# Kernel tuning notes

Hardware: AMD Instinct MI355X
Metric: run time of the kernel (lower is better)

Reference implementation:

```python
import jax, jax.numpy as jnp
import numpy as np

D, H, DFF, NE, ND, B = 512, 8, 2048, 64, 64, 16

def _ln(x, g, b):
    m = x.mean(-1, keepdims=True)
    v = ((x - m) ** 2).mean(-1, keepdims=True)
    return (x - m) * jax.lax.rsqrt(v + 1e-5) * g + b

def _mha(q, k, v, Wi, bi, Wo, bo, h=H):
    # q,k,v: (L, B, d) seq-first, like torch nn.MultiheadAttention (eval mode)
    Lq, Bb, d = q.shape
    hd = d // h
    Wq, Wk, Wv = jnp.split(Wi, 3, axis=0)
    bq, bk, bv = jnp.split(bi, 3)
    def proj(x, W, bb):
        y = x @ W.T + bb                                  # (L, B, d)
        return y.reshape(x.shape[0], Bb, h, hd).transpose(1, 2, 0, 3)  # (B, h, L, hd)
    qh = proj(q, Wq, bq) * (hd ** -0.5)
    kh = proj(k, Wk, bk)
    vh = proj(v, Wv, bv)
    a = jax.nn.softmax(jnp.einsum('bhqe,bhke->bhqk', qh, kh), axis=-1)
    o = jnp.einsum('bhqk,bhke->bhqe', a, vh).transpose(2, 0, 1, 3).reshape(Lq, Bb, d)
    return o @ Wo.T + bo

def _ffn(x, W1, b1, W2, b2):
    return jax.nn.relu(x @ W1.T + b1) @ W2.T + b2

def _forward(enc, dec, ec_Wi, ec_bi, ec_Wo, ec_bo, dc_Wi, dc_bi, dc_Wo, dc_bo,
             es_Wi, es_bi, es_Wo, es_bo, ds_Wi, ds_bi, ds_Wo, ds_bo,
             eff_W1, eff_b1, eff_W2, eff_b2, dff_W1, dff_b1, dff_W2, dff_b2,
             n_ec_g, n_ec_b, n_es_g, n_es_b, n_ef_g, n_ef_b, n_dc_g, n_dc_b,
             n_dci_g, n_dci_b, n_ds_g, n_ds_b, n_df_g, n_df_b, pW, pWb, pv, pb):
    f_n = _ln(enc, n_ec_g, n_ec_b)   # (ne, B, d) -- normed once, reused for all j
    G_n = _ln(dec, n_dc_g, n_dc_b)   # (nd, B, d)
    # dec_cross for all j at once (key/value is the single token f_j)
    dc_out = jax.vmap(lambda fj: _mha(G_n, fj[None], fj[None], dc_Wi, dc_bi, dc_Wo, dc_bo))(f_n)  # (ne, nd, B, d)
    G_fj = dec[None] + dc_out                            # (ne, nd, B, d)
    G_im = _ln(G_fj, n_dci_g, n_dci_b)
    # enc_cross for all j at once (query is the single token f_j)
    ec_out = jax.vmap(lambda fj, Gj: _mha(fj[None], Gj, Gj, ec_Wi, ec_bi, ec_Wo, ec_bo)[0])(f_n, G_im)  # (ne, B, d)
    enc1 = enc + ec_out
    # attention pooling over the ne fusion copies
    G_c = G_fj.transpose(2, 1, 0, 3)                     # (B, nd, ne, d)
    energy = jnp.tanh(G_c @ pW.T + pWb + pb)
    w = jax.nn.softmax(energy @ pv.T, axis=2)            # (B, nd, ne, 1)
    dec1 = (G_c * w).sum(axis=2).transpose(1, 0, 2)      # (nd, B, d)
    # self-attention + FFN (pre-norm residual)
    en = _ln(enc1, n_es_g, n_es_b)
    enc2 = enc1 + _mha(en, en, en, es_Wi, es_bi, es_Wo, es_bo)
    dn = _ln(dec1, n_ds_g, n_ds_b)
    dec2 = dec1 + _mha(dn, dn, dn, ds_Wi, ds_bi, ds_Wo, ds_bo)
    enc3 = enc2 + _ffn(_ln(enc2, n_ef_g, n_ef_b), eff_W1, eff_b1, eff_W2, eff_b2)
    dec3 = dec2 + _ffn(_ln(dec2, n_df_g, n_df_b), dff_W1, dff_b1, dff_W2, dff_b2)
    return (enc3, dec3)

def setup_inputs() -> dict:
    key = jax.random.key(0)
    ks = iter(jax.random.split(key, 64))
    def w(shape, scale=0.05):
        return jax.random.normal(next(ks), shape, jnp.float32) * scale
    d, dff = D, DFF
    inp = {
        'enc': jax.random.normal(next(ks), (NE, B, d), jnp.float32),
        'dec': jax.random.normal(next(ks), (ND, B, d), jnp.float32),
    }
    for p in ['ec', 'dc', 'es', 'ds']:
        inp[p + '_Wi'] = w((3 * d, d)); inp[p + '_bi'] = jnp.zeros(3 * d, jnp.float32)
        inp[p + '_Wo'] = w((d, d)); inp[p + '_bo'] = jnp.zeros(d, jnp.float32)
    for p in ['eff', 'dff']:
        inp[p + '_W1'] = w((dff, d)); inp[p + '_b1'] = jnp.zeros(dff, jnp.float32)
        inp[p + '_W2'] = w((d, dff)); inp[p + '_b2'] = jnp.zeros(d, jnp.float32)
    for p in ['n_ec', 'n_es', 'n_ef', 'n_dc', 'n_dci', 'n_ds', 'n_df']:
        inp[p + '_g'] = jnp.ones(d, jnp.float32); inp[p + '_b'] = jnp.zeros(d, jnp.float32)
    inp['pW'] = w((d, d)); inp['pWb'] = jnp.zeros(d, jnp.float32)
    inp['pv'] = w((1, d)); inp['pb'] = jnp.zeros(d, jnp.float32)
    return inp

def reference(enc, dec, ec_Wi, ec_bi, ec_Wo, ec_bo, dc_Wi, dc_bi, dc_Wo, dc_bo,
              es_Wi, es_bi, es_Wo, es_bo, ds_Wi, ds_bi, ds_Wo, ds_bo,
              eff_W1, eff_b1, eff_W2, eff_b2, dff_W1, dff_b1, dff_W2, dff_b2,
              n_ec_g, n_ec_b, n_es_g, n_es_b, n_ef_g, n_ef_b, n_dc_g, n_dc_b,
              n_dci_g, n_dci_b, n_ds_g, n_ds_b, n_df_g, n_df_b, pW, pWb, pv, pb):
    return _forward(enc, dec, ec_Wi, ec_bi, ec_Wo, ec_bo, dc_Wi, dc_bi, dc_Wo, dc_bo,
                    es_Wi, es_bi, es_Wo, es_bo, ds_Wi, ds_bi, ds_Wo, ds_bo,
                    eff_W1, eff_b1, eff_W2, eff_b2, dff_W1, dff_b1, dff_W2, dff_b2,
                    n_ec_g, n_ec_b, n_es_g, n_es_b, n_ef_g, n_ef_b, n_dc_g, n_dc_b,
                    n_dci_g, n_dci_b, n_ds_g, n_ds_b, n_df_g, n_df_b, pW, pWb, pv, pb)
```

## Files before the change

### kernel.cpp

```cpp
#include <hip/hip_runtime.h>


typedef __bf16 bf16_t;
typedef bf16_t bf16x8 __attribute__((ext_vector_type(8)));
typedef float f32x4 __attribute__((ext_vector_type(4)));
typedef unsigned short u16x4 __attribute__((ext_vector_type(4)));
typedef unsigned short u16x8 __attribute__((ext_vector_type(8)));

__device__ inline unsigned short f2bf(float f) {
  unsigned int u = __float_as_uint(f);
  u += 0x7fffu + ((u >> 16) & 1u);
  return (unsigned short)(u >> 16);
}
__device__ inline float bf2f(unsigned short u) {
  return __uint_as_float(((unsigned int)u) << 16);
}

__device__ inline float wsum(float v) {
#pragma unroll
  for (int o = 1; o < 64; o <<= 1) v += __shfl_xor(v, o);
  return v;
}
__device__ inline float wmax(float v) {
#pragma unroll
  for (int o = 1; o < 64; o <<= 1) v = fmaxf(v, __shfl_xor(v, o));
  return v;
}

struct CastJob {
  const float* src;
  unsigned short* dst;
  int n;
  const float* cs;
};
struct CastPage {
  const float* src;
  unsigned short* dst;
};

__device__ inline void ln_body(const float* __restrict__ x,
                               const float* __restrict__ g,
                               const float* __restrict__ be,
                               unsigned short* __restrict__ y, int t) {
  float2 v = *(const float2*)(x + 2 * t);
  float s = wsum(v.x + v.y);
  float s2 = wsum(v.x * v.x + v.y * v.y);
  __shared__ float sh[8];
  int w = t >> 6, lane = t & 63;
  if (lane == 0) { sh[w] = s; sh[4 + w] = s2; }
  __syncthreads();
  s = sh[0] + sh[1] + sh[2] + sh[3];
  s2 = sh[4] + sh[5] + sh[6] + sh[7];
  float mean = s * (1.f / 512.f);
  float var = s2 * (1.f / 512.f) - mean * mean;
  float r = rsqrtf(var + 1e-5f);
  float2 gg = *(const float2*)(g + 2 * t);
  float2 bb = *(const float2*)(be + 2 * t);
  unsigned int pk = (unsigned int)f2bf((v.x - mean) * r * gg.x + bb.x) |
                    ((unsigned int)f2bf((v.y - mean) * r * gg.y + bb.y) << 16);
  *(unsigned int*)(y + 2 * t) = pk;
}

__device__ inline void stats_body(const float* __restrict__ x,
                                  float* __restrict__ m, float* __restrict__ q2,
                                  unsigned short* __restrict__ xb, int t,
                                  int row) {
  float2 v = *(const float2*)(x + 2 * t);
  if (xb) {
    unsigned int pk = (unsigned int)f2bf(v.x) | ((unsigned int)f2bf(v.y) << 16);
    *(unsigned int*)(xb + 2 * t) = pk;
  }
  float s = wsum(v.x + v.y);
  float s2 = wsum(v.x * v.x + v.y * v.y);
  __shared__ float sh2[8];
  int w = t >> 6, lane = t & 63;
  if (lane == 0) { sh2[w] = s; sh2[4 + w] = s2; }
  __syncthreads();
  if (t == 0) {
    s = sh2[0] + sh2[1] + sh2[2] + sh2[3];
    s2 = sh2[4] + sh2[5] + sh2[6] + sh2[7];
    m[row] = s * (1.f / 512.f);
    q2[row] = s2 * (1.f / 512.f);
  }
}

struct Phase0Args {
  const float* enc; const float* g_ec; const float* b_ec; unsigned short* f_n;
  const float* dec; float* md; float* q2d; unsigned short* dec_b;
  CastJob cast[4];
  const float* Wk; const float* Wv; const float* bk; const float* bv;
  const float* g_dci; const float* b_dci;
  float* u_k; float* u_v; float* c_k; float* c_v;
  const float* WoA; const float* WvA; unsigned short* Wfb;
  const float* bv2; const float* bo2; float* bf_out;
  float* zbase; int zcount;
};

__global__ __launch_bounds__(256) void phase0(Phase0Args a) {
  __shared__ unsigned short WAs[64][72];
  __shared__ unsigned short WBs[64][72];
  int bx = blockIdx.x;
  const int t = threadIdx.x;
  if (bx < 64) {
    const int bm = (bx >> 3) * 64;
    const int bn = (bx & 7) * 64;
    const int lane = t & 63;
    const int wave = t >> 6;
    const int wr = wave >> 1;
    const int wc = wave & 1;
    const int fr = lane & 15;
    const int fg = lane >> 4;
    const int rr = t >> 2;
    const int c = (t & 3) * 16;
    f32x4 acc[2][2] = {};
    for (int m0 = 0; m0 < 512; m0 += 64) {
      const float* ap = a.WoA + (size_t)(bm + rr) * 512 + m0 + c;
      float4 a0 = *(const float4*)ap;
      float4 a1 = *(const float4*)(ap + 4);
      float4 a2 = *(const float4*)(ap + 8);
      float4 a3 = *(const float4*)(ap + 12);
      u16x8 lo = {f2bf(a0.x), f2bf(a0.y), f2bf(a0.z), f2bf(a0.w),
                  f2bf(a1.x), f2bf(a1.y), f2bf(a1.z), f2bf(a1.w)};
      u16x8 hi = {f2bf(a2.x), f2bf(a2.y), f2bf(a2.z), f2bf(a2.w),
                  f2bf(a3.x), f2bf(a3.y), f2bf(a3.z), f2bf(a3.w)};
      *(u16x8*)&WAs[rr][c] = lo;
      *(u16x8*)&WAs[rr][c + 8] = hi;
      const float* bp = a.WvA + (size_t)(m0 + rr) * 512 + bn + c;
      float4 b0 = *(const float4*)bp;
      float4 b1 = *(const float4*)(bp + 4);
      float4 b2 = *(const float4*)(bp + 8);
      float4 b3 = *(const float4*)(bp + 12);
      float bv16[16] = {b0.x, b0.y, b0.z, b0.w, b1.x, b1.y, b1.z, b1.w,
                        b2.x, b2.y, b2.z, b2.w, b3.x, b3.y, b3.z, b3.w};
#pragma unroll
      for (int jj = 0; jj < 16; ++jj) WBs[c + jj][rr] = f2bf(bv16[jj]);
      __syncthreads();
#pragma unroll
      for (int ks = 0; ks < 2; ++ks) {
        int kk = ks * 32 + fg * 8;
        bf16x8 fa0 = *(const bf16x8*)&WAs[wr * 32 + fr][kk];
        bf16x8 fa1 = *(const bf16x8*)&WAs[wr * 32 + 16 + fr][kk];
        bf16x8 fb0 = *(const bf16x8*)&WBs[wc * 32 + fr][kk];
        bf16x8 fb1 = *(const bf16x8*)&WBs[wc * 32 + 16 + fr][kk];
        acc[0][0] = __builtin_amdgcn_mfma_f32_16x16x32_bf16(fa0, fb0, acc[0][0], 0, 0, 0);
        acc[0][1] = __builtin_amdgcn_mfma_f32_16x16x32_bf16(fa0, fb1, acc[0][1], 0, 0, 0);
        acc[1][0] = __builtin_amdgcn_mfma_f32_16x16x32_bf16(fa1, fb0, acc[1][0], 0, 0, 0);
        acc[1][1] = __builtin_amdgcn_mfma_f32_16x16x32_bf16(fa1, fb1, acc[1][1], 0, 0, 0);
      }
      __syncthreads();
    }
#pragma unroll
    for (int mt = 0; mt < 2; ++mt) {
#pragma unroll
      for (int nt = 0; nt < 2; ++nt) {
        int col = bn + wc * 32 + nt * 16 + fr;
        int rowb = bm + wr * 32 + mt * 16 + fg * 4;
#pragma unroll
        for (int r = 0; r < 4; ++r) {
          a.Wfb[(size_t)(rowb + r) * 512 + col] = f2bf(acc[mt][nt][r]);
        }
      }
    }
    return;
  }
  bx -= 64;
  if (bx < 2048) {
    int row = bx;
    if (row < 1024) {
      ln_body(a.enc + (size_t)row * 512, a.g_ec, a.b_ec,
              a.f_n + (size_t)row * 512, t);
    } else {
      row -= 1024;
      stats_body(a.dec + (size_t)row * 512, a.md, a.q2d,
                 a.dec_b + (size_t)row * 512, t, row);
    }
    return;
  }
  bx -= 2048;
  if (bx < 256) {
    int e = ((bx << 8) | t) << 4;
    int jj = e >> 18;
    int i = e & 262143;
    const CastJob cj = a.cast[jj];
    const float* s = cj.src + i;
    float4 v0 = *(const float4*)s;
    float4 v1 = *(const float4*)(s + 4);
    float4 v2 = *(const float4*)(s + 8);
    float4 v3 = *(const float4*)(s + 12);
    if (cj.cs) {
      int k = i & 511;
      float4 c0 = *(const float4*)(cj.cs + k);
      float4 c1 = *(const float4*)(cj.cs + k + 4);
      float4 c2 = *(const float4*)(cj.cs + k + 8);
      float4 c3 = *(const float4*)(cj.cs + k + 12);
      v0.x *= c0.x; v0.y *= c0.y; v0.z *= c0.z; v0.w *= c0.w;
      v1.x *= c1.x; v1.y *= c1.y; v1.z *= c1.z; v1.w *= c1.w;
      v2.x *= c2.x; v2.y *= c2.y; v2.z *= c2.z; v2.w *= c2.w;
      v3.x *= c3.x; v3.y *= c3.y; v3.z *= c3.z; v3.w *= c3.w;
    }
    u16x8 o0 = {f2bf(v0.x), f2bf(v0.y), f2bf(v0.z), f2bf(v0.w),
                f2bf(v1.x), f2bf(v1.y), f2bf(v1.z), f2bf(v1.w)};
    u16x8 o1 = {f2bf(v2.x), f2bf(v2.y), f2bf(v2.z), f2bf(v2.w),
                f2bf(v3.x), f2bf(v3.y), f2bf(v3.z), f2bf(v3.w)};
    *(u16x8*)(cj.dst + i) = o0;
    *(u16x8*)(cj.dst + i + 8) = o1;
    return;
  }
  bx -= 256;
  if (bx < 128) {
    int n = bx * 4 + (t >> 6);
    int lane = t & 63;
    const float* wk = a.Wk + (size_t)n * 512;
    const float* wv = a.Wv + (size_t)n * 512;
    const float* wo = a.WoA + (size_t)n * 512;
    float uk = 0.f, uv = 0.f, ck = 0.f, cv = 0.f, bfa = 0.f;
#pragma unroll
    for (int k0 = 0; k0 < 512; k0 += 64) {
      int k = k0 + lane;
      float x = wk[k], y = wv[k], gg = a.g_dci[k], bb = a.b_dci[k];
      uk += x * gg; ck += x * bb;
      uv += y * gg; cv += y * bb;
      bfa += wo[k] * a.bv2[k];
    }
    uk = wsum(uk); uv = wsum(uv); ck = wsum(ck); cv = wsum(cv);
    bfa = wsum(bfa);
    if (lane == 0) {
      a.u_k[n] = uk; a.u_v[n] = uv;
      a.c_k[n] = ck + a.bk[n]; a.c_v[n] = cv + a.bv[n];
      a.bf_out[n] = bfa + a.bo2[n];
    }
    return;
  }
  for (int i = t; i < a.zcount; i += 256) a.zbase[i] = 0.f;
}

struct GemmJob {
  const unsigned short* X;
  const float* Xf;
  const float* Asum; const float* Asq;
  const float* g; const float* be;
  const unsigned short* W;
  const float* bias;
  const float* resid;
  float* Y;
  unsigned short* Ybf;
  float* Ssum; float* Ssq;
  float scale;
  int relu;
};
struct MrJob {
  const unsigned short* A; const unsigned short* B;
  const float* md; const float* q2d;
  const float* ts; const float* tsq;
  float* mArr; float* rArr;
};
struct PoolJob {
  const float* Ed; const float* Et; const float* pv; const float* dec;
  const unsigned short* tbf; float* dec1; float* d1s; float* d1q;
};
struct GemmBatch {
  GemmJob j[5];
  MrJob mr;
  CastPage cp[25];
  int cast_total;
  PoolJob pl;
};

__device__ inline u16x8 fold_pack(float4 va, float4 vb, const float* gp,
                                  const float* bp, float m, float ri) {
  float4 g0 = *(const float4*)gp;
  float4 g1 = *(const float4*)(gp + 4);
  float4 e0 = *(const float4*)bp;
  float4 e1 = *(const float4*)(bp + 4);
  u16x8 o;
  o[0] = f2bf((va.x - m) * ri * g0.x + e0.x);
  o[1] = f2bf((va.y - m) * ri * g0.y + e0.y);
  o[2] = f2bf((va.z - m) * ri * g0.z + e0.z);
  o[3] = f2bf((va.w - m) * ri * g0.w + e0.w);
  o[4] = f2bf((vb.x - m) * ri * g1.x + e1.x);
  o[5] = f2bf((vb.y - m) * ri * g1.y + e1.y);
  o[6] = f2bf((vb.z - m) * ri * g1.z + e1.z);
  o[7] = f2bf((vb.w - m) * ri * g1.w + e1.w);
  return o;
}

__device__ void pool_body(const PoolJob& p, int i, int b) {
  __shared__ float esh[64], wsh[64], pps[8];
  const int t = threadIdx.x;
  int wave = t >> 6, lane = t & 63;
  const float* ed = p.Ed + (size_t)(i * 16 + b) * 512;
  float4 ea = *(const float4*)(ed + lane * 8);
  float4 eb = *(const float4*)(ed + lane * 8 + 4);
  float4 pa = *(const float4*)(p.pv + lane * 8);
  float4 pb4 = *(const float4*)(p.pv + lane * 8 + 4);
  float edv[8] = {ea.x, ea.y, ea.z, ea.w, eb.x, eb.y, eb.z, eb.w};
  float pvv[8] = {pa.x, pa.y, pa.z, pa.w, pb4.x, pb4.y, pb4.z, pb4.w};
#pragma unroll 4
  for (int jl = 0; jl < 16; ++jl) {
    int j = wave * 16 + jl;
    const float* et = p.Et + (size_t)(j * 16 + b) * 512;
    float4 ta = *(const float4*)(et + lane * 8);
    float4 tb4 = *(const float4*)(et + lane * 8 + 4);
    float etv[8] = {ta.x, ta.y, ta.z, ta.w, tb4.x, tb4.y, tb4.z, tb4.w};
    float s = 0.f;
#pragma unroll
    for (int c = 0; c < 8; ++c) {
      float x = edv[c] + etv[c];
      float e2 = __expf(2.f * x);
      float th = 1.f - 2.f * __builtin_amdgcn_rcpf(e2 + 1.f);
      s += th * pvv[c];
    }
    s = wsum(s);
    if (lane == 0) esh[j] = s;
  }
  __syncthreads();
  if (t < 64) {
    float e = esh[t];
    float mx = wmax(e);
    float ex = __expf(e - mx);
    float se = wsum(ex);
    wsh[t] = ex / se;
  }
  __syncthreads();
  size_t rowib = (size_t)(i * 16 + b) * 512;
  int d2 = t * 2;
  float2 dv = *(const float2*)(p.dec + rowib + d2);
  float acc0 = dv.x, acc1 = dv.y;
#pragma unroll 16
  for (int j2 = 0; j2 < 64; ++j2) {
    const unsigned short* tp = p.tbf + (size_t)(j2 * 16 + b) * 512 + d2;
    float w = wsh[j2];
    acc0 += w * bf2f(tp[0]);
    acc1 += w * bf2f(tp[1]);
  }
  float2 ov = {acc0, acc1};
  *(float2*)(p.dec1 + rowib + d2) = ov;
  float s1 = acc0 + acc1;
  float s2v = acc0 * acc0 + acc1 * acc1;
  s1 = wsum(s1);
  s2v = wsum(s2v);
  if (lane == 0) { pps[wave] = s1; pps[4 + wave] = s2v; }
  __syncthreads();
  if (t == 0) {
    p.d1s[i * 16 + b] = pps[0] + pps[1] + pps[2] + pps[3];
    p.d1q[i * 16 + b] = pps[4] + pps[5] + pps[6] + pps[7];
  }
}

template <int EXTRA, bool FOLD, bool STATS, int NW, int BMT>
__global__ __launch_bounds__(NW * 64) void gemm_bf16(GemmBatch gb, int M,
                                                     int N, int K, int xz) {
  const int t = threadIdx.x;
  constexpr int NT = NW * 64;
  if constexpr (EXTRA == 1) {
    if ((int)blockIdx.z >= xz) {
      const int nbz = (int)(gridDim.x * gridDim.y);
      const int bid = ((int)blockIdx.z - xz) * nbz +
                      (int)blockIdx.y * (int)gridDim.x + (int)blockIdx.x;
      const int nthr = ((int)gridDim.z - xz) * nbz * NT;
      for (int base = (bid * NT + t) * 16; base < gb.cast_total;
           base += nthr * 16) {
        int page = base >> 18;
        int off = base & 262143;
        const float* s = gb.cp[page].src + off;
        unsigned short* d = gb.cp[page].dst + off;
        float4 v0 = *(const float4*)s;
        float4 v1 = *(const float4*)(s + 4);
        float4 v2 = *(const float4*)(s + 8);
        float4 v3 = *(const float4*)(s + 12);
        u16x8 o0 = {f2bf(v0.x), f2bf(v0.y), f2bf(v0.z), f2bf(v0.w),
                    f2bf(v1.x), f2bf(v1.y), f2bf(v1.z), f2bf(v1.w)};
        u16x8 o1 = {f2bf(v2.x), f2bf(v2.y), f2bf(v2.z), f2bf(v2.w),
                    f2bf(v3.x), f2bf(v3.y), f2bf(v3.z), f2bf(v3.w)};
        *(u16x8*)d = o0;
        *(u16x8*)(d + 8) = o1;
      }
      return;
    }
  }
  if constexpr (EXTRA == 3) {
    if ((int)blockIdx.z >= xz) {
      int pb = ((int)blockIdx.z - xz) * (int)(gridDim.x * gridDim.y) +
               (int)blockIdx.y * (int)gridDim.x + (int)blockIdx.x;
      pool_body(gb.pl, pb & 63, pb >> 6);
      return;
    }
  }
  __shared__ unsigned short As[BMT][72];
  __shared__ unsigned short Bs[64][72];
  const int lane = t & 63;
  const int wave = t >> 6;
  const int wr = wave >> 1;
  const int wc = wave & 1;
  const int fr = lane & 15;
  const int fg = lane >> 4;
  constexpr int MT = (NW == 4 || BMT == 128) ? 2 : 1;
  constexpr int RB = MT * 16;
  const int r0 = t >> 3, o0 = (t & 7) * 8;
  const int r1 = ((t + 256) >> 3) & 63, o1 = ((t + 256) & 7) * 8;

  if constexpr (EXTRA == 2) {
    if ((int)blockIdx.z == xz) {
      const int bb = blockIdx.y * gridDim.x + blockIdx.x;
      if (bb >= 16) return;
      const unsigned short* Ap = gb.mr.A + (size_t)bb * 512;
      const unsigned short* Bp = gb.mr.B + (size_t)bb * 512;
      f32x4 acc[2][2] = {};
      for (int k0 = 0; k0 < 512; k0 += 64) {
        *(u16x8*)&As[r0][o0] = *(const u16x8*)&Ap[(size_t)r0 * 8192 + k0 + o0];
        *(u16x8*)&As[r1][o1] = *(const u16x8*)&Ap[(size_t)r1 * 8192 + k0 + o1];
        *(u16x8*)&Bs[r0][o0] = *(const u16x8*)&Bp[(size_t)r0 * 8192 + k0 + o0];
        *(u16x8*)&Bs[r1][o1] = *(const u16x8*)&Bp[(size_t)r1 * 8192 + k0 + o1];
        __syncthreads();
#pragma unroll
        for (int ks = 0; ks < 2; ++ks) {
          int kk = ks * 32 + fg * 8;
          bf16x8 a0 = *(const bf16x8*)&As[wr * 32 + fr][kk];
          bf16x8 a1 = *(const bf16x8*)&As[wr * 32 + 16 + fr][kk];
          bf16x8 b0 = *(const bf16x8*)&Bs[wc * 32 + fr][kk];
          bf16x8 b1 = *(const bf16x8*)&Bs[wc * 32 + 16 + fr][kk];
          acc[0][0] = __builtin_amdgcn_mfma_f32_16x16x32_bf16(a0, b0, acc[0][0], 0, 0, 0);
          acc[0][1] = __builtin_amdgcn_mfma_f32_16x16x32_bf16(a0, b1, acc[0][1], 0, 0, 0);
          acc[1][0] = __builtin_amdgcn_mfma_f32_16x16x32_bf16(a1, b0, acc[1][0], 0, 0, 0);
          acc[1][1] = __builtin_amdgcn_mfma_f32_16x16x32_bf16(a1, b1, acc[1][1], 0, 0, 0);
        }
        __syncthreads();
      }
#pragma unroll
      for (int nt = 0; nt < 2; ++nt) {
        int j = wc * 32 + nt * 16 + fr;
        float mtv = gb.mr.ts[j * 16 + bb] * (1.f / 512.f);
        float qtv = gb.mr.tsq[j * 16 + bb] * (1.f / 512.f);
#pragma unroll
        for (int mt = 0; mt < 2; ++mt) {
          int ibase = wr * 32 + mt * 16 + fg * 4;
#pragma unroll
          for (int r = 0; r < 4; ++r) {
            int i = ibase + r;
            float s = acc[mt][nt][r];
            float mean = gb.mr.md[i * 16 + bb] + mtv;
            float msq = gb.mr.q2d[i * 16 + bb] + qtv + s * (2.f / 512.f);
            int idx = bb * 4096 + j * 64 + i;
            gb.mr.mArr[idx] = mean;
            gb.mr.rArr[idx] = rsqrtf(msq - mean * mean + 1e-5f);
          }
        }
      }
      return;
    }
  }

  const GemmJob jb = gb.j[blockIdx.z];
  int flat = (int)blockIdx.y * (int)gridDim.x + (int)blockIdx.x;
  {
    const int nwg = (int)(gridDim.x * gridDim.y);
    flat = (flat & 7) * (nwg >> 3) + (flat >> 3);
  }
  const int bm = (flat / (int)gridDim.x) * BMT;
  const int bn = (flat % (int)gridDim.x) * 64;
  f32x4 acc[MT][2] = {};
  const unsigned short* Wp = jb.W + (size_t)bn * K;
  const int ra = (NW == 4) ? r1 : r0 + 64;
  const int oa = (NW == 4) ? o1 : o0;

  u16x8 xa0, xa1;
  float4 fa0a, fa0b, fa1a, fa1b;
  float lm0 = 0.f, lr0i = 0.f, lm1 = 0.f, lr1i = 0.f;
  const unsigned short* Xp = nullptr;
  constexpr bool A2 = (NW == 4) || (BMT == 128);
  if constexpr (FOLD) {
    float s = jb.Asum[bm + r0], q = jb.Asq[bm + r0];
    lm0 = s * (1.f / 512.f);
    lr0i = rsqrtf(q * (1.f / 512.f) - lm0 * lm0 + 1e-5f);
    if constexpr (A2) {
      s = jb.Asum[bm + ra]; q = jb.Asq[bm + ra];
      lm1 = s * (1.f / 512.f);
      lr1i = rsqrtf(q * (1.f / 512.f) - lm1 * lm1 + 1e-5f);
    }
    const float* p0 = jb.Xf + (size_t)(bm + r0) * K + o0;
    fa0a = *(const float4*)p0; fa0b = *(const float4*)(p0 + 4);
    if constexpr (A2) {
      const float* p1 = jb.Xf + (size_t)(bm + ra) * K + oa;
      fa1a = *(const float4*)p1; fa1b = *(const float4*)(p1 + 4);
    }
  } else {
    Xp = jb.X + (size_t)bm * K;
    xa0 = *(const u16x8*)&Xp[(size_t)r0 * K + o0];
    if constexpr (A2) xa1 = *(const u16x8*)&Xp[(size_t)ra * K + oa];
  }
  u16x8 wa0 = *(const u16x8*)&Wp[(size_t)r0 * K + o0];
  u16x8 wa1;
  if constexpr (NW == 4) wa1 = *(const u16x8*)&Wp[(size_t)r1 * K + o1];

  for (int k0 = 0; k0 < K; k0 += 64) {
    if constexpr (FOLD) {
      *(u16x8*)&As[r0][o0] = fold_pack(fa0a, fa0b, jb.g + k0 + o0, jb.be + k0 + o0, lm0, lr0i);
      if constexpr (A2)
        *(u16x8*)&As[ra][oa] = fold_pack(fa1a, fa1b, jb.g + k0 + oa, jb.be + k0 + oa, lm1, lr1i);
    } else {
      *(u16x8*)&As[r0][o0] = xa0;
      if constexpr (A2) *(u16x8*)&As[ra][oa] = xa1;
    }
    *(u16x8*)&Bs[r0][o0] = wa0;
    if constexpr (NW == 4) *(u16x8*)&Bs[r1][o1] = wa1;
    __syncthreads();
    if (k0 + 64 < K) {
      const int kn = k0 + 64;
      if constexpr (FOLD) {
        const float* p0 = jb.Xf + (size_t)(bm + r0) * K + kn + o0;
        fa0a = *(const float4*)p0; fa0b = *(const float4*)(p0 + 4);
        if constexpr (A2) {
          const float* p1 = jb.Xf + (size_t)(bm + ra) * K + kn + oa;
          fa1a = *(const float4*)p1; fa1b = *(const float4*)(p1 + 4);
        }
      } else {
        xa0 = *(const u16x8*)&Xp[(size_t)r0 * K + kn + o0];
        if constexpr (A2) xa1 = *(const u16x8*)&Xp[(size_t)ra * K + kn + oa];
      }
      wa0 = *(const u16x8*)&Wp[(size_t)r0 * K + kn + o0];
      if constexpr (NW == 4) wa1 = *(const u16x8*)&Wp[(size_t)r1 * K + kn + o1];
    }
#pragma unroll
    for (int ks = 0; ks < 2; ++ks) {
      int kk = ks * 32 + fg * 8;
      bf16x8 b0 = *(const bf16x8*)&Bs[wc * 32 + fr][kk];
      bf16x8 b1 = *(const bf16x8*)&Bs[wc * 32 + 16 + fr][kk];
      if constexpr (MT == 2) {
        bf16x8 a0 = *(const bf16x8*)&As[wr * 32 + fr][kk];
        bf16x8 a1 = *(const bf16x8*)&As[wr * 32 + 16 + fr][kk];
        acc[0][0] = __builtin_amdgcn_mfma_f32_16x16x32_bf16(a0, b0, acc[0][0], 0, 0, 0);
        acc[0][1] = __builtin_amdgcn_mfma_f32_16x16x32_bf16(a0, b1, acc[0][1], 0, 0, 0);
        acc[1][0] = __builtin_amdgcn_mfma_f32_16x16x32_bf16(a1, b0, acc[1][0], 0, 0, 0);
        acc[1][1] = __builtin_amdgcn_mfma_f32_16x16x32_bf16(a1, b1, acc[1][1], 0, 0, 0);
      } else {
        bf16x8 a0 = *(const bf16x8*)&As[wr * 16 + fr][kk];
        acc[0][0] = __builtin_amdgcn_mfma_f32_16x16x32_bf16(a0, b0, acc[0][0], 0, 0, 0);
        acc[0][1] = __builtin_amdgcn_mfma_f32_16x16x32_bf16(a0, b1, acc[0][1], 0, 0, 0);
      }
    }
    __syncthreads();
  }
  float rsum[MT][4], rsq[MT][4];
  if constexpr (STATS) {
#pragma unroll
    for (int mt = 0; mt < MT; ++mt)
#pragma unroll
      for (int r = 0; r < 4; ++r) { rsum[mt][r] = 0.f; rsq[mt][r] = 0.f; }
  }
#pragma unroll
  for (int mt = 0; mt < MT; ++mt) {
#pragma unroll
    for (int nt = 0; nt < 2; ++nt) {
      int col = bn + wc * 32 + nt * 16 + fr;
      int rowb = bm + wr * RB + mt * 16 + fg * 4;
      float bia = jb.bias ? jb.bias[col] : 0.f;
#pragma unroll
      for (int r = 0; r < 4; ++r) {
        float v = (acc[mt][nt][r] + bia) * jb.scale;
        if (jb.relu) v = fmaxf(v, 0.f);
        if (jb.resid) v += jb.resid[(size_t)(rowb + r) * N + col];
        size_t idx = (size_t)(rowb + r) * N + col;
        if (jb.Y) jb.Y[idx] = v;
        if (jb.Ybf) jb.Ybf[idx] = f2bf(v);
        if constexpr (STATS) { rsum[mt][r] += v; rsq[mt][r] += v * v; }
      }
    }
  }
  if constexpr (STATS) {
    if (jb.Ssum) {
#pragma unroll
      for (int mt = 0; mt < MT; ++mt)
#pragma unroll
        for (int r = 0; r < 4; ++r) {
          float s = rsum[mt][r], q = rsq[mt][r];
#pragma unroll
          for (int o = 1; o < 16; o <<= 1) {
            s += __shfl_xor(s, o);
            q += __shfl_xor(q, o);
          }
          if (fr == 0) {
            int row = bm + wr * RB + mt * 16 + fg * 4 + r;
            atomicAdd(&jb.Ssum[row], s);
            atomicAdd(&jb.Ssq[row], q);
          }
        }
    }
  }
}

__global__ __launch_bounds__(128) void ec_attn(
    const unsigned short* __restrict__ Qe, const unsigned short* __restrict__ Kd,
    const unsigned short* __restrict__ Kt, const unsigned short* __restrict__ Vd,
    const unsigned short* __restrict__ Vt, const float* __restrict__ u_k,
    const float* __restrict__ u_v, const float* __restrict__ c_k,
    const float* __restrict__ c_v, const float* __restrict__ mArr,
    const float* __restrict__ rArr, unsigned short* __restrict__ O) {
  int bx = blockIdx.x;
  int h = bx & 7;
  int b = (bx >> 3) & 15;
  int jlo = (bx >> 7) * 32;
  __shared__ unsigned short Qs[32][72];
  __shared__ unsigned short Ks[64][72];
  __shared__ unsigned short VdT[64][72];
  __shared__ unsigned short Ps[32][72];
  __shared__ float stp[32][4], sup[32][4], scp[32][4];
  __shared__ float stv[32], suv[32], scv[32], swv[32], swmv[32];
  int t = threadIdx.x;
  int wave = t >> 6, lane = t & 63;
  int fr = lane & 15, fg = lane >> 4;
  {
    int row = t >> 2;
    int qt = t & 3;
    int cb = qt * 16;
    size_t base = (size_t)((jlo + row) * 16 + b) * 512 + h * 64 + cb;
    u16x8 q0 = *(const u16x8*)(Qe + base);
    u16x8 q1 = *(const u16x8*)(Qe + base + 8);
    u16x8 kt0 = *(const u16x8*)(Kt + base);
    u16x8 kt1 = *(const u16x8*)(Kt + base + 8);
    *(u16x8*)&Qs[row][cb] = q0;
    *(u16x8*)&Qs[row][cb + 8] = q1;
    float st_ = 0.f, su_ = 0.f, sc_ = 0.f;
#pragma unroll
    for (int jj = 0; jj < 8; ++jj) {
      float qa = bf2f(q0[jj]), qb = bf2f(q1[jj]);
      st_ += qa * bf2f(kt0[jj]) + qb * bf2f(kt1[jj]);
      su_ += qa * u_k[h * 64 + cb + jj] + qb * u_k[h * 64 + cb + 8 + jj];
      sc_ += qa * c_k[h * 64 + cb + jj] + qb * c_k[h * 64 + cb + 8 + jj];
    }
    stp[row][qt] = st_;
    sup[row][qt] = su_;
    scp[row][qt] = sc_;
    int row2 = t >> 1;
    int c0 = (t & 1) * 32;
    size_t base2 = (size_t)(row2 * 16 + b) * 512 + h * 64 + c0;
    u16x8 k0 = *(const u16x8*)(Kd + base2);
    u16x8 k1 = *(const u16x8*)(Kd + base2 + 8);
    u16x8 k2 = *(const u16x8*)(Kd + base2 + 16);
    u16x8 k3 = *(const u16x8*)(Kd + base2 + 24);
    u16x8 v0 = *(const u16x8*)(Vd + base2);
    u16x8 v1 = *(const u16x8*)(Vd + base2 + 8);
    u16x8 v2 = *(const u16x8*)(Vd + base2 + 16);
    u16x8 v3 = *(const u16x8*)(Vd + base2 + 24);
    *(u16x8*)&Ks[row2][c0] = k0;
    *(u16x8*)&Ks[row2][c0 + 8] = k1;
    *(u16x8*)&Ks[row2][c0 + 16] = k2;
    *(u16x8*)&Ks[row2][c0 + 24] = k3;
#pragma unroll
    for (int jj = 0; jj < 8; ++jj) VdT[c0 + jj][row2] = v0[jj];
#pragma unroll
    for (int jj = 0; jj < 8; ++jj) VdT[c0 + 8 + jj][row2] = v1[jj];
#pragma unroll
    for (int jj = 0; jj < 8; ++jj) VdT[c0 + 16 + jj][row2] = v2[jj];
#pragma unroll
    for (int jj = 0; jj < 8; ++jj) VdT[c0 + 24 + jj][row2] = v3[jj];
  }
  float mv[4][4], rv[4][4], vtv[4][4], uvv[4], cvv[4];
#pragma unroll
  for (int r = 0; r < 4; ++r) {
    int gj = jlo + wave * 16 + fg * 4 + r;
    const float* mrow = mArr + (size_t)b * 4096 + gj * 64;
    const float* rrow = rArr + (size_t)b * 4096 + gj * 64;
#pragma unroll
    for (int c = 0; c < 4; ++c) {
      mv[r][c] = mrow[c * 16 + fr];
      rv[r][c] = rrow[c * 16 + fr];
    }
  }
#pragma unroll
  for (int nt = 0; nt < 4; ++nt) {
    int d = nt * 16 + fr;
    uvv[nt] = u_v[h * 64 + d];
    cvv[nt] = c_v[h * 64 + d];
#pragma unroll
    for (int r = 0; r < 4; ++r) {
      int gj = jlo + wave * 16 + fg * 4 + r;
      vtv[nt][r] = bf2f(Vt[(size_t)(gj * 16 + b) * 512 + h * 64 + d]);
    }
  }
  __syncthreads();
  if (t < 32) {
    stv[t] = stp[t][0] + stp[t][1] + stp[t][2] + stp[t][3];
    suv[t] = sup[t][0] + sup[t][1] + sup[t][2] + sup[t][3];
    scv[t] = scp[t][0] + scp[t][1] + scp[t][2] + scp[t][3];
  }
  __syncthreads();
  f32x4 sacc[4] = {};
  bf16x8 aq0 = *(const bf16x8*)&Qs[wave * 16 + fr][fg * 8];
  bf16x8 aq1 = *(const bf16x8*)&Qs[wave * 16 + fr][32 + fg * 8];
#pragma unroll
  for (int nt = 0; nt < 4; ++nt) {
    bf16x8 b0 = *(const bf16x8*)&Ks[nt * 16 + fr][fg * 8];
    bf16x8 b1 = *(const bf16x8*)&Ks[nt * 16 + fr][32 + fg * 8];
    sacc[nt] = __builtin_amdgcn_mfma_f32_16x16x32_bf16(aq0, b0, sacc[nt], 0, 0, 0);
    sacc[nt] = __builtin_amdgcn_mfma_f32_16x16x32_bf16(aq1, b1, sacc[nt], 0, 0, 0);
  }
#pragma unroll
  for (int r = 0; r < 4; ++r) {
    int lj = wave * 16 + fg * 4 + r;
    float stj = stv[lj], suj = suv[lj], scj = scv[lj];
    float a0 = rv[r][0] * (sacc[0][r] + stj - mv[r][0] * suj) + scj;
    float a1 = rv[r][1] * (sacc[1][r] + stj - mv[r][1] * suj) + scj;
    float a2 = rv[r][2] * (sacc[2][r] + stj - mv[r][2] * suj) + scj;
    float a3 = rv[r][3] * (sacc[3][r] + stj - mv[r][3] * suj) + scj;
    float mx = fmaxf(fmaxf(a0, a1), fmaxf(a2, a3));
#pragma unroll
    for (int o = 1; o < 16; o <<= 1) mx = fmaxf(mx, __shfl_xor(mx, o));
    a0 = __expf(a0 - mx);
    a1 = __expf(a1 - mx);
    a2 = __expf(a2 - mx);
    a3 = __expf(a3 - mx);
    float se = a0 + a1 + a2 + a3;
#pragma unroll
    for (int o = 1; o < 16; o <<= 1) se += __shfl_xor(se, o);
    float inv = 1.f / se;
    float w0 = a0 * inv * rv[r][0];
    float w1 = a1 * inv * rv[r][1];
    float w2 = a2 * inv * rv[r][2];
    float w3 = a3 * inv * rv[r][3];
    float sw = w0 + w1 + w2 + w3;
    float swm = w0 * mv[r][0] + w1 * mv[r][1] + w2 * mv[r][2] + w3 * mv[r][3];
#pragma unroll
    for (int o = 1; o < 16; o <<= 1) {
      sw += __shfl_xor(sw, o);
      swm += __shfl_xor(swm, o);
    }
    Ps[lj][fr] = f2bf(w0);
    Ps[lj][16 + fr] = f2bf(w1);
    Ps[lj][32 + fr] = f2bf(w2);
    Ps[lj][48 + fr] = f2bf(w3);
    if (fr == 0) {
      swv[lj] = sw;
      swmv[lj] = swm;
    }
  }
  f32x4 oc[4] = {};
  bf16x8 ap0 = *(const bf16x8*)&Ps[wave * 16 + fr][fg * 8];
  bf16x8 ap1 = *(const bf16x8*)&Ps[wave * 16 + fr][32 + fg * 8];
#pragma unroll
  for (int nt = 0; nt < 4; ++nt) {
    bf16x8 b0 = *(const bf16x8*)&VdT[nt * 16 + fr][fg * 8];
    bf16x8 b1 = *(const bf16x8*)&VdT[nt * 16 + fr][32 + fg * 8];
    oc[nt] = __builtin_amdgcn_mfma_f32_16x16x32_bf16(ap0, b0, oc[nt], 0, 0, 0);
    oc[nt] = __builtin_amdgcn_mfma_f32_16x16x32_bf16(ap1, b1, oc[nt], 0, 0, 0);
  }
#pragma unroll
  for (int nt = 0; nt < 4; ++nt) {
    int d = nt * 16 + fr;
#pragma unroll
    for (int r = 0; r < 4; ++r) {
      int lj = wave * 16 + fg * 4 + r;
      int gj = jlo + lj;
      size_t gidx = (size_t)(gj * 16 + b) * 512 + h * 64 + d;
      float o = oc[nt][r] + swv[lj] * vtv[nt][r] - swmv[lj] * uvv[nt] + cvv[nt];
      O[gidx] = f2bf(o);
    }
  }
}

__global__ __launch_bounds__(128) void self_attn(
    const unsigned short* __restrict__ QKVe, unsigned short* __restrict__ Oe,
    const unsigned short* __restrict__ QKVd, unsigned short* __restrict__ Od) {
  const unsigned short* QKV = blockIdx.z ? QKVd : QKVe;
  unsigned short* O = blockIdx.z ? Od : Oe;
  int h = blockIdx.x & 7;
  int b = blockIdx.x >> 3;
  int qlo = blockIdx.y * 32;
  __shared__ unsigned short Qs[32][72];
  __shared__ unsigned short Ksh[64][72];
  __shared__ unsigned short VT[64][72];
  __shared__ unsigned short Ps[32][72];
  int t = threadIdx.x;
  {
    int row = t >> 2;
    int cb = (t & 3) * 16;
    const unsigned short* src =
        QKV + (size_t)((qlo + row) * 16 + b) * 1536 + h * 64 + cb;
    u16x8 q0 = *(const u16x8*)(src);
    u16x8 q1 = *(const u16x8*)(src + 8);
    *(u16x8*)&Qs[row][cb] = q0;
    *(u16x8*)&Qs[row][cb + 8] = q1;
    int row2 = t >> 1;
    int c0 = (t & 1) * 32;
    const unsigned short* src2 =
        QKV + (size_t)(row2 * 16 + b) * 1536 + h * 64 + c0;
    u16x8 k0 = *(const u16x8*)(src2 + 512);
    u16x8 k1 = *(const u16x8*)(src2 + 520);
    u16x8 k2 = *(const u16x8*)(src2 + 528);
    u16x8 k3 = *(const u16x8*)(src2 + 536);
    u16x8 v0 = *(const u16x8*)(src2 + 1024);
    u16x8 v1 = *(const u16x8*)(src2 + 1032);
    u16x8 v2 = *(const u16x8*)(src2 + 1040);
    u16x8 v3 = *(const u16x8*)(src2 + 1048);
    *(u16x8*)&Ksh[row2][c0] = k0;
    *(u16x8*)&Ksh[row2][c0 + 8] = k1;
    *(u16x8*)&Ksh[row2][c0 + 16] = k2;
    *(u16x8*)&Ksh[row2][c0 + 24] = k3;
#pragma unroll
    for (int jj = 0; jj < 8; ++jj) VT[c0 + jj][row2] = v0[jj];
#pragma unroll
    for (int jj = 0; jj < 8; ++jj) VT[c0 + 8 + jj][row2] = v1[jj];
#pragma unroll
    for (int jj = 0; jj < 8; ++jj) VT[c0 + 16 + jj][row2] = v2[jj];
#pragma unroll
    for (int jj = 0; jj < 8; ++jj) VT[c0 + 24 + jj][row2] = v3[jj];
  }
  __syncthreads();
  int wave = t >> 6, lane = t & 63;
  int fr = lane & 15, fg = lane >> 4;
  f32x4 sc[4] = {};
  bf16x8 aq0 = *(const bf16x8*)&Qs[wave * 16 + fr][fg * 8];
  bf16x8 aq1 = *(const bf16x8*)&Qs[wave * 16 + fr][32 + fg * 8];
#pragma unroll
  for (int nt = 0; nt < 4; ++nt) {
    bf16x8 b0 = *(const bf16x8*)&Ksh[nt * 16 + fr][fg * 8];
    bf16x8 b1 = *(const bf16x8*)&Ksh[nt * 16 + fr][32 + fg * 8];
    sc[nt] = __builtin_amdgcn_mfma_f32_16x16x32_bf16(aq0, b0, sc[nt], 0, 0, 0);
    sc[nt] = __builtin_amdgcn_mfma_f32_16x16x32_bf16(aq1, b1, sc[nt], 0, 0, 0);
  }
#pragma unroll
  for (int r = 0; r < 4; ++r) {
    float a0 = sc[0][r] * 0.125f, a1 = sc[1][r] * 0.125f;
    float a2 = sc[2][r] * 0.125f, a3 = sc[3][r] * 0.125f;
    float mx = fmaxf(fmaxf(a0, a1), fmaxf(a2, a3));
#pragma unroll
    for (int o = 1; o < 16; o <<= 1) mx = fmaxf(mx, __shfl_xor(mx, o));
    a0 = __expf(a0 - mx);
    a1 = __expf(a1 - mx);
    a2 = __expf(a2 - mx);
    a3 = __expf(a3 - mx);
    float se = a0 + a1 + a2 + a3;
#pragma unroll
    for (int o = 1; o < 16; o <<= 1) se += __shfl_xor(se, o);
    float inv = 1.f / se;
    int prow = wave * 16 + fg * 4 + r;
    Ps[prow][0 + fr] = f2bf(a0 * inv);
    Ps[prow][16 + fr] = f2bf(a1 * inv);
    Ps[prow][32 + fr] = f2bf(a2 * inv);
    Ps[prow][48 + fr] = f2bf(a3 * inv);
  }
  f32x4 oc[4] = {};
  bf16x8 ap0 = *(const bf16x8*)&Ps[wave * 16 + fr][fg * 8];
  bf16x8 ap1 = *(const bf16x8*)&Ps[wave * 16 + fr][32 + fg * 8];
#pragma unroll
  for (int nt = 0; nt < 4; ++nt) {
    bf16x8 b0 = *(const bf16x8*)&VT[nt * 16 + fr][fg * 8];
    bf16x8 b1 = *(const bf16x8*)&VT[nt * 16 + fr][32 + fg * 8];
    oc[nt] = __builtin_amdgcn_mfma_f32_16x16x32_bf16(ap0, b0, oc[nt], 0, 0, 0);
    oc[nt] = __builtin_amdgcn_mfma_f32_16x16x32_bf16(ap1, b1, oc[nt], 0, 0, 0);
  }
#pragma unroll
  for (int nt = 0; nt < 4; ++nt) {
#pragma unroll
    for (int r = 0; r < 4; ++r) {
      int q = qlo + wave * 16 + fg * 4 + r;
      int d = nt * 16 + fr;
      O[(size_t)(q * 16 + b) * 512 + h * 64 + d] = f2bf(oc[nt][r]);
    }
  }
}

extern "C" void kernel_launch(void* const* d_in, const int* in_sizes, int n_in,
                              void* d_out, int out_size, void* d_ws,
                              size_t ws_size, hipStream_t stream) {
  const float* enc = (const float*)d_in[0];
  const float* dec = (const float*)d_in[1];
  const float* ec_Wi = (const float*)d_in[2];
  const float* ec_bi = (const float*)d_in[3];
  const float* ec_Wo = (const float*)d_in[4];
  const float* ec_bo = (const float*)d_in[5];
  const float* dc_Wi = (const float*)d_in[6];
  const float* dc_bi = (const float*)d_in[7];
  const float* dc_Wo = (const float*)d_in[8];
  const float* dc_bo = (const float*)d_in[9];
  const float* es_Wi = (const float*)d_in[10];
  const float* es_bi = (const float*)d_in[11];
  const float* es_Wo = (const float*)d_in[12];
  const float* es_bo = (const float*)d_in[13];
  const float* ds_Wi = (const float*)d_in[14];
  const float* ds_bi = (const float*)d_in[15];
  const float* ds_Wo = (const float*)d_in[16];
  const float* ds_bo = (const float*)d_in[17];
  const float* eff_W1 = (const float*)d_in[18];
  const float* eff_b1 = (const float*)d_in[19];
  const float* eff_W2 = (const float*)d_in[20];
  const float* eff_b2 = (const float*)d_in[21];
  const float* dff_W1 = (const float*)d_in[22];
  const float* dff_b1 = (const float*)d_in[23];
  const float* dff_W2 = (const float*)d_in[24];
  const float* dff_b2 = (const float*)d_in[25];
  const float* n_ec_g = (const float*)d_in[26];
  const float* n_ec_b = (const float*)d_in[27];
  const float* n_es_g = (const float*)d_in[28];
  const float* n_es_b = (const float*)d_in[29];
  const float* n_ef_g = (const float*)d_in[30];
  const float* n_ef_b = (const float*)d_in[31];
  const float* n_dci_g = (const float*)d_in[34];
  const float* n_dci_b = (const float*)d_in[35];
  const float* n_ds_g = (const float*)d_in[36];
  const float* n_ds_b = (const float*)d_in[37];
  const float* n_df_g = (const float*)d_in[38];
  const float* n_df_b = (const float*)d_in[39];
  const float* pW = (const float*)d_in[40];
  const float* pWb = (const float*)d_in[41];
  const float* pv = (const float*)d_in[42];
  const float* pb = (const float*)d_in[43];

  float* ws = (float*)d_ws;
  const size_t U = 524288;
  float* Ed = ws + 3 * U;
  float* Et = ws + 7 * U;
  float* enc1 = ws + 8 * U;
  float* dec1 = ws + 9 * U;
  float* enc2 = ws + 10 * U;
  float* dec2 = ws + 11 * U;
  float* sm = ws + 12 * U;
  float* md = sm;
  float* q2d = sm + 1024;
  float* bf = sm + 2048;
  float* u_k = sm + 4096;
  float* u_v = sm + 4608;
  float* c_k = sm + 5120;
  float* c_v = sm + 5632;
  float* mArr = sm + 6144;
  float* rArr = sm + 6144 + 65536;
  float* stx = ws + 24 * U;
  float* t_s = stx;
  float* t_sq = stx + 1024;
  float* e1s = stx + 2048;
  float* e1q = stx + 3072;
  float* d1s = stx + 4096;
  float* d1q = stx + 5120;
  float* e2s = stx + 6144;
  float* e2q = stx + 7168;
  float* d2s = stx + 8192;
  float* d2q = stx + 9216;
  unsigned short* ub0 = (unsigned short*)ws;
  unsigned short* Qe_b = ub0 + 0 * U;
  unsigned short* Kd_b = ub0 + 1 * U;
  unsigned short* Vd_b = ub0 + 2 * U;
  unsigned short* Kt_b = ub0 + 3 * U;
  unsigned short* Vt_b = ub0 + 4 * U;
  unsigned short* ub = (unsigned short*)(ws + 12 * U + 137216);
  const int W262 = 262144, W786 = 786432, W1M = 1048576;
  unsigned short* w_Wf = ub;
  unsigned short* w_ecWq = w_Wf + W262;
  unsigned short* w_ecWkg = w_ecWq + W262;
  unsigned short* w_ecWvg = w_ecWkg + W262;
  unsigned short* w_pW = w_ecWvg + W262;
  unsigned short* w_unused = w_pW + W262;
  unsigned short* w_ecWo = w_unused + W262;
  unsigned short* w_esWi = w_ecWo + W262;
  unsigned short* w_dsWi = w_esWi + W786;
  unsigned short* w_esWo = w_dsWi + W786;
  unsigned short* w_dsWo = w_esWo + W262;
  unsigned short* w_effW1 = w_dsWo + W262;
  unsigned short* w_dffW1 = w_effW1 + W1M;
  unsigned short* w_effW2 = w_dffW1 + W1M;
  unsigned short* w_dffW2 = w_effW2 + W1M;
  unsigned short* actb = w_dffW2 + W1M;
  unsigned short* f_n_b = actb;
  unsigned short* dec_b = actb + 2 * U;
  unsigned short* tb_b = actb + 3 * U;
  unsigned short* Oec_b = actb + 4 * U;
  unsigned short* OaE = dec_b;
  unsigned short* OaD = tb_b;
  unsigned short* QKVe_b = (unsigned short*)(ws + 0 * U);
  unsigned short* QKVd_b = (unsigned short*)(ws + 2 * U);
  unsigned short* He_b = (unsigned short*)(ws + 0 * U);
  unsigned short* Hd_b = (unsigned short*)(ws + 2 * U);

  const float* dc_Wv = dc_Wi + 1024 * 512;
  const float* dc_bv = dc_bi + 1024;
  const float* ec_Wq = ec_Wi;
  const float* ec_bq = ec_bi;
  const float* ec_Wk = ec_Wi + 512 * 512;
  const float* ec_bk = ec_bi + 512;
  const float* ec_Wv = ec_Wi + 1024 * 512;
  const float* ec_bv = ec_bi + 1024;

  auto J = [](const unsigned short* X, const unsigned short* W,
              const float* bias, const float* resid, float* Y,
              unsigned short* Ybf, float scale, int relu) {
    GemmJob j{};
    j.X = X; j.W = W; j.bias = bias; j.resid = resid;
    j.Y = Y; j.Ybf = Ybf; j.scale = scale; j.relu = relu;
    return j;
  };
  auto JF = [](const float* Xf, const float* As, const float* Aq,
               const float* g, const float* be, const unsigned short* W,
               const float* bias, unsigned short* Ybf, int relu) {
    GemmJob j{};
    j.Xf = Xf; j.Asum = As; j.Asq = Aq; j.g = g; j.be = be;
    j.W = W; j.bias = bias; j.Ybf = Ybf; j.scale = 1.f; j.relu = relu;
    return j;
  };

  {
    Phase0Args pa{};
    pa.enc = enc; pa.g_ec = n_ec_g; pa.b_ec = n_ec_b; pa.f_n = f_n_b;
    pa.dec = dec; pa.md = md; pa.q2d = q2d; pa.dec_b = dec_b;
    pa.cast[0] = {ec_Wq, w_ecWq, W262, nullptr};
    pa.cast[1] = {ec_Wk, w_ecWkg, W262, n_dci_g};
    pa.cast[2] = {ec_Wv, w_ecWvg, W262, n_dci_g};
    pa.cast[3] = {pW, w_pW, W262, nullptr};
    pa.Wk = ec_Wk; pa.Wv = ec_Wv; pa.bk = ec_bk; pa.bv = ec_bv;
    pa.g_dci = n_dci_g; pa.b_dci = n_dci_b;
    pa.u_k = u_k; pa.u_v = u_v; pa.c_k = c_k; pa.c_v = c_v;
    pa.WoA = dc_Wo; pa.WvA = dc_Wv; pa.Wfb = w_Wf;
    pa.bv2 = dc_bv; pa.bo2 = dc_bo; pa.bf_out = bf;
    pa.zbase = stx; pa.zcount = 10240;
    phase0<<<2497, 256, 0, stream>>>(pa);
  }
  {
    GemmBatch gb{};
    gb.j[0] = J(f_n_b, w_Wf, bf, nullptr, nullptr, tb_b, 1.f, 0);
    gb.j[0].Ssum = t_s; gb.j[0].Ssq = t_sq;
    gb.j[1] = J(f_n_b, w_ecWq, ec_bq, nullptr, nullptr, Qe_b, 0.125f, 0);
    gb.j[2] = J(dec_b, w_ecWkg, nullptr, nullptr, nullptr, Kd_b, 1.f, 0);
    gb.j[3] = J(dec_b, w_ecWvg, nullptr, nullptr, nullptr, Vd_b, 1.f, 0);
    gb.j[4] = J(dec_b, w_pW, pWb, nullptr, Ed, nullptr, 1.f, 0);
    int pg = 0;
    auto addpages = [&](const float* s, unsigned short* d, int n) {
      for (int off = 0; off < n; off += W262) {
        gb.cp[pg].src = s + off;
        gb.cp[pg].dst = d + off;
        ++pg;
      }
    };
    addpages(ec_Wo, w_ecWo, W262);
    addpages(es_Wi, w_esWi, W786);
    addpages(ds_Wi, w_dsWi, W786);
    addpages(es_Wo, w_esWo, W262);
    addpages(ds_Wo, w_dsWo, W262);
    addpages(eff_W1, w_effW1, W1M);
    addpages(dff_W1, w_dffW1, W1M);
    addpages(eff_W2, w_effW2, W1M);
    addpages(dff_W2, w_dffW2, W1M);
    gb.cast_total = pg * W262;
    gemm_bf16<1, false, true, 8, 128><<<dim3(8, 8, 7), 512, 0, stream>>>(
        gb, 1024, 512, 512, 5);
  }
  {
    GemmBatch gb{};
    gb.j[0] = J(tb_b, w_ecWkg, nullptr, nullptr, nullptr, Kt_b, 1.f, 0);
    gb.j[1] = J(tb_b, w_ecWvg, nullptr, nullptr, nullptr, Vt_b, 1.f, 0);
    gb.j[2] = J(tb_b, w_pW, pb, nullptr, Et, nullptr, 1.f, 0);
    gb.mr = {dec_b, tb_b, md, q2d, t_s, t_sq, mArr, rArr};
    gemm_bf16<2, false, false, 4, 64><<<dim3(8, 16, 4), 256, 0, stream>>>(
        gb, 1024, 512, 512, 3);
  }
  ec_attn<<<256, 128, 0, stream>>>(Qe_b, Kd_b, Kt_b, Vd_b, Vt_b, u_k, u_v, c_k,
                                   c_v, mArr, rArr, Oec_b);
  {
    GemmBatch gb{};
    gb.j[0] = J(Oec_b, w_ecWo, ec_bo, enc, enc1, nullptr, 1.f, 0);
    gb.j[0].Ssum = e1s; gb.j[0].Ssq = e1q;
    gb.pl = {Ed, Et, pv, dec, tb_b, dec1, d1s, d1q};
    gemm_bf16<3, false, true, 4, 64><<<dim3(8, 16, 9), 256, 0, stream>>>(
        gb, 1024, 512, 512, 1);
  }
  {
    GemmBatch gb{};
    gb.j[0] = JF(enc1, e1s, e1q, n_es_g, n_es_b, w_esWi, es_bi, QKVe_b, 0);
    gb.j[1] = JF(dec1, d1s, d1q, n_ds_g, n_ds_b, w_dsWi, ds_bi, QKVd_b, 0);
    gemm_bf16<0, true, false, 8, 128><<<dim3(24, 8, 2), 512, 0, stream>>>(
        gb, 1024, 1536, 512, -1);
  }
  self_attn<<<dim3(128, 2, 2), 128, 0, stream>>>(QKVe_b, OaE, QKVd_b, OaD);
  {
    GemmBatch gb{};
    gb.j[0] = J(OaE, w_esWo, es_bo, enc1, enc2, nullptr, 1.f, 0);
    gb.j[0].Ssum = e2s; gb.j[0].Ssq = e2q;
    gb.j[1] = J(OaD, w_dsWo, ds_bo, dec1, dec2, nullptr, 1.f, 0);
    gb.j[1].Ssum = d2s; gb.j[1].Ssq = d2q;
    gemm_bf16<0, false, true, 8, 64><<<dim3(8, 16, 2), 512, 0, stream>>>(
        gb, 1024, 512, 512, -1);
  }
  {
    GemmBatch gb{};
    gb.j[0] = JF(enc2, e2s, e2q, n_ef_g, n_ef_b, w_effW1, eff_b1, He_b, 1);
    gb.j[1] = JF(dec2, d2s, d2q, n_df_g, n_df_b, w_dffW1, dff_b1, Hd_b, 1);
    gemm_bf16<0, true, false, 8, 128><<<dim3(32, 8, 2), 512, 0, stream>>>(
        gb, 1024, 2048, 512, -1);
  }
  float* out = (float*)d_out;
  {
    GemmBatch gb{};
    gb.j[0] = J(He_b, w_effW2, eff_b2, enc2, out, nullptr, 1.f, 0);
    gb.j[1] = J(Hd_b, w_dffW2, dff_b2, dec2, out + U, nullptr, 1.f, 0);
    gemm_bf16<0, false, false, 8, 64><<<dim3(8, 16, 2), 512, 0, stream>>>(
        gb, 1024, 512, 2048, -1);
  }
}
```

Before: 286.7 us.

## Move attention-pooling blocks from ec_Wo GEMM launch into ec_attn launch

The attention-pooling work (1024 blocks) was appended as extra blocks of the ec output-projection GEMM and is now appended to the ec_attn launch instead. The pooling body is rewritten for 128-thread blocks, with each wave handling 32 energies and each thread accumulating 4 columns using vector loads. This lets pooling overlap with the small 256-block ec_attn grid rather than the GEMM, and shrinks the GEMM launch. The risk is that ec_attn's larger shared-memory footprint limits occupancy for the pooling blocks, and each pooling block now does twice as much work per thread.

```diff
diff --git a/kernel.cpp b/kernel.cpp
--- a/kernel.cpp
+++ b/kernel.cpp
@@ -263,7 +263,6 @@
   MrJob mr;
   CastPage cp[25];
   int cast_total;
-  PoolJob pl;
 };
 
 __device__ inline u16x8 fold_pack(float4 va, float4 vb, const float* gp,
@@ -284,8 +283,8 @@
   return o;
 }
 
-__device__ void pool_body(const PoolJob& p, int i, int b) {
-  __shared__ float esh[64], wsh[64], pps[8];
+__device__ void pool_body128(const PoolJob& p, int i, int b) {
+  __shared__ float esh[64], wsh[64], pps2[4];
   const int t = threadIdx.x;
   int wave = t >> 6, lane = t & 63;
   const float* ed = p.Ed + (size_t)(i * 16 + b) * 512;
@@ -296,8 +295,8 @@
   float edv[8] = {ea.x, ea.y, ea.z, ea.w, eb.x, eb.y, eb.z, eb.w};
   float pvv[8] = {pa.x, pa.y, pa.z, pa.w, pb4.x, pb4.y, pb4.z, pb4.w};
 #pragma unroll 4
-  for (int jl = 0; jl < 16; ++jl) {
-    int j = wave * 16 + jl;
+  for (int jl = 0; jl < 32; ++jl) {
+    int j = wave * 32 + jl;
     const float* et = p.Et + (size_t)(j * 16 + b) * 512;
     float4 ta = *(const float4*)(et + lane * 8);
     float4 tb4 = *(const float4*)(et + lane * 8 + 4);
@@ -323,27 +322,30 @@
   }
   __syncthreads();
   size_t rowib = (size_t)(i * 16 + b) * 512;
-  int d2 = t * 2;
-  float2 dv = *(const float2*)(p.dec + rowib + d2);
-  float acc0 = dv.x, acc1 = dv.y;
+  int d4 = t * 4;
+  float4 dv = *(const float4*)(p.dec + rowib + d4);
+  float acc0 = dv.x, acc1 = dv.y, acc2 = dv.z, acc3 = dv.w;
 #pragma unroll 16
   for (int j2 = 0; j2 < 64; ++j2) {
-    const unsigned short* tp = p.tbf + (size_t)(j2 * 16 + b) * 512 + d2;
+    const unsigned short* tp = p.tbf + (size_t)(j2 * 16 + b) * 512 + d4;
+    u16x4 tv = *(const u16x4*)tp;
     float w = wsh[j2];
-    acc0 += w * bf2f(tp[0]);
-    acc1 += w * bf2f(tp[1]);
-  }
-  float2 ov = {acc0, acc1};
-  *(float2*)(p.dec1 + rowib + d2) = ov;
-  float s1 = acc0 + acc1;
-  float s2v = acc0 * acc0 + acc1 * acc1;
+    acc0 += w * bf2f(tv[0]);
+    acc1 += w * bf2f(tv[1]);
+    acc2 += w * bf2f(tv[2]);
+    acc3 += w * bf2f(tv[3]);
+  }
+  float4 ov = {acc0, acc1, acc2, acc3};
+  *(float4*)(p.dec1 + rowib + d4) = ov;
+  float s1 = acc0 + acc1 + acc2 + acc3;
+  float s2v = acc0 * acc0 + acc1 * acc1 + acc2 * acc2 + acc3 * acc3;
   s1 = wsum(s1);
   s2v = wsum(s2v);
-  if (lane == 0) { pps[wave] = s1; pps[4 + wave] = s2v; }
+  if (lane == 0) { pps2[wave] = s1; pps2[2 + wave] = s2v; }
   __syncthreads();
   if (t == 0) {
-    p.d1s[i * 16 + b] = pps[0] + pps[1] + pps[2] + pps[3];
-    p.d1q[i * 16 + b] = pps[4] + pps[5] + pps[6] + pps[7];
+    p.d1s[i * 16 + b] = pps2[0] + pps2[1];
+    p.d1q[i * 16 + b] = pps2[2] + pps2[3];
   }
 }
 
@@ -378,14 +380,6 @@
       return;
     }
   }
-  if constexpr (EXTRA == 3) {
-    if ((int)blockIdx.z >= xz) {
-      int pb = ((int)blockIdx.z - xz) * (int)(gridDim.x * gridDim.y) +
-               (int)blockIdx.y * (int)gridDim.x + (int)blockIdx.x;
-      pool_body(gb.pl, pb & 63, pb >> 6);
-      return;
-    }
-  }
   __shared__ unsigned short As[BMT][72];
   __shared__ unsigned short Bs[64][72];
   const int lane = t & 63;
@@ -594,8 +588,14 @@
     const unsigned short* __restrict__ Vt, const float* __restrict__ u_k,
     const float* __restrict__ u_v, const float* __restrict__ c_k,
     const float* __restrict__ c_v, const float* __restrict__ mArr,
-    const float* __restrict__ rArr, unsigned short* __restrict__ O) {
+    const float* __restrict__ rArr, unsigned short* __restrict__ O,
+    PoolJob pl) {
   int bx = blockIdx.x;
+  if (bx >= 256) {
+    int pb = bx - 256;
+    pool_body128(pl, pb & 63, pb >> 6);
+    return;
+  }
   int h = bx & 7;
   int b = (bx >> 3) & 15;
   int jlo = (bx >> 7) * 32;
@@ -1049,15 +1049,17 @@
     gemm_bf16<2, false, false, 4, 64><<<dim3(8, 16, 4), 256, 0, stream>>>(
         gb, 1024, 512, 512, 3);
   }
-  ec_attn<<<256, 128, 0, stream>>>(Qe_b, Kd_b, Kt_b, Vd_b, Vt_b, u_k, u_v, c_k,
-                                   c_v, mArr, rArr, Oec_b);
+  {
+    PoolJob pl = {Ed, Et, pv, dec, tb_b, dec1, d1s, d1q};
+    ec_attn<<<1280, 128, 0, stream>>>(Qe_b, Kd_b, Kt_b, Vd_b, Vt_b, u_k, u_v,
+                                      c_k, c_v, mArr, rArr, Oec_b, pl);
+  }
   {
     GemmBatch gb{};
     gb.j[0] = J(Oec_b, w_ecWo, ec_bo, enc, enc1, nullptr, 1.f, 0);
     gb.j[0].Ssum = e1s; gb.j[0].Ssq = e1q;
-    gb.pl = {Ed, Et, pv, dec, tb_b, dec1, d1s, d1q};
-    gemm_bf16<3, false, true, 4, 64><<<dim3(8, 16, 9), 256, 0, stream>>>(
-        gb, 1024, 512, 512, 1);
+    gemm_bf16<0, false, true, 4, 64><<<dim3(8, 16, 1), 256, 0, stream>>>(
+        gb, 1024, 512, 512, -1);
   }
   {
     GemmBatch gb{};
```

New measurement: 302.1 us. 5.3% more time.
